# Kernel optimization log

Measured on AMD Instinct MI355X. Metric: run time of the kernel, lower is better.

Reference implementation:

```python
import jax, jax.numpy as jnp
import numpy as np

TAU = 1.0
BETA = 0.1
MIN_NORM = 1.0
B = 4194304


def setup_inputs() -> dict:
    key = jax.random.key(0)
    # positions spread over the four-well landscape (minima near (0.5+-1, 0.5+-1))
    batch = jax.random.normal(key, (B, 2), dtype=jnp.float32) * 1.5
    return {"batch": batch}


def reference(batch):
    batch = batch.reshape(-1, 2)
    u = batch[..., 0] - 0.5
    v = batch[..., 1] - 0.5

    # potential V4 = (u^2-1)^2 + (v^2-1)^2 + beta*u*v
    energy = (u * u - 1.0) ** 2 + (v * v - 1.0) ** 2 + BETA * u * v

    # analytic gradient, forces = -grad
    gx = 4.0 * u * (u * u - 1.0) + BETA * v
    gy = 4.0 * v * (v * v - 1.0) + BETA * u
    forces = -jnp.stack((gx, gy), axis=-1)  # (B, 2)

    # analytic Hessian (B, 2, 2)
    hxx = 12.0 * (u * u) - 4.0
    hyy = 12.0 * (v * v) - 4.0
    hxy = jnp.full_like(hxx, BETA)
    hessian = jnp.stack(
        (jnp.stack((hxx, hxy), axis=-1), jnp.stack((hxy, hyy), axis=-1)), axis=-2
    )

    # eigh: ascending eigenvalues, matching torch.linalg.eigh convention
    eigenvals, eigenvecs = jnp.linalg.eigh(hessian)
    smallest_eigvec = eigenvecs[..., :, 0]  # (B, 2)

    # GAD direction: reflect forces along smallest-eigenvalue eigenvector
    gad = -forces + 2.0 * jnp.sum(forces * smallest_eigvec, axis=-1, keepdims=True) * smallest_eigvec

    # norm_gad_outside_ts branch: normalize gad outside saddle region if small
    eigval_product = eigenvals[..., 0] * eigenvals[..., 1]
    gad_mag = jnp.linalg.norm(gad, axis=-1, keepdims=True)  # (B, 1)
    mask = (eigval_product > 0) & (gad_mag[..., 0] < MIN_NORM)
    gad = jnp.where(mask[..., None], gad / jnp.maximum(gad_mag, 1e-30), gad)

    energy_grad = gad / TAU
    return energy, forces, energy_grad, hessian, eigenvals[..., 0], eigenvals[..., 1]
```

## Files before the change

### kernel.cpp

```cpp
#include <hip/hip_runtime.h>


typedef float f2v __attribute__((ext_vector_type(2)));
typedef float f4v __attribute__((ext_vector_type(4)));

namespace {

__device__ __forceinline__ f2v mk2(float a, float b) {
    f2v r; r.x = a; r.y = b; return r;
}
__device__ __forceinline__ f4v mk4(float a, float b, float c, float d) {
    f4v r; r.x = a; r.y = b; r.z = c; r.w = d; return r;
}

struct PointOut {
    float e, fx, fy, gx, gy, hxx, hyy, l0, l1;
};

__device__ __forceinline__ PointOut compute_point(float px, float py) {
    const float BETA = 0.1f;
    PointOut o;
    float u = px - 0.5f;
    float v = py - 0.5f;
    float uu = u * u;
    float vv = v * v;
    float a = uu - 1.0f;
    float b = vv - 1.0f;

    o.e = a * a + b * b + BETA * u * v;

    float gx = 4.0f * u * a + BETA * v;
    float gy = 4.0f * v * b + BETA * u;
    o.fx = -gx;
    o.fy = -gy;

    o.hxx = 12.0f * uu - 4.0f;
    o.hyy = 12.0f * vv - 4.0f;

    float d = 0.5f * (o.hxx - o.hyy);
    float m = 0.5f * (o.hxx + o.hyy);
    float r = sqrtf(d * d + BETA * BETA);
    o.l0 = m - r;
    o.l1 = m + r;

    bool pos = (d >= 0.0f);
    float wx = pos ? BETA : (d - r);
    float wy = pos ? -(d + r) : BETA;
    float n2 = wx * wx + wy * wy;

    float fd = o.fx * wx + o.fy * wy;
    float s = 2.0f * fd / n2;
    float gadx = -o.fx + s * wx;
    float gady = -o.fy + s * wy;

    float prod = o.l0 * o.l1;
    float gmag = sqrtf(gadx * gadx + gady * gady);
    float scale = (prod > 0.0f && gmag < 1.0f)
                      ? (1.0f / fmaxf(gmag, 1e-30f))
                      : 1.0f;
    o.gx = gadx * scale;
    o.gy = gady * scale;
    return o;
}

}

__global__ __launch_bounds__(256) void fw_energy_gad_kernel(
    const f2v* __restrict__ in, float* __restrict__ out, int n) {
    const float BETA = 0.1f;
    int half = n >> 1;
    size_t N = (size_t)n;
    size_t H = (size_t)half;

    float* e_out  = out;
    f2v*   f_out  = (f2v*)(out + N);
    f2v*   g_out  = (f2v*)(out + 3 * N);
    f4v*   h_out  = (f4v*)(out + 5 * N);
    float* l0_out = out + 9 * N;
    float* l1_out = out + 10 * N;

    int i = blockIdx.x * blockDim.x + threadIdx.x;
    if (i < half) {
        f2v p0 = in[i];
        f2v p1 = in[i + H];
        PointOut o0 = compute_point(p0.x, p0.y);
        PointOut o1 = compute_point(p1.x, p1.y);

        __builtin_nontemporal_store(o0.e, e_out + i);
        __builtin_nontemporal_store(o1.e, e_out + i + H);
        __builtin_nontemporal_store(mk2(o0.fx, o0.fy), f_out + i);
        __builtin_nontemporal_store(mk2(o1.fx, o1.fy), f_out + i + H);
        __builtin_nontemporal_store(mk2(o0.gx, o0.gy), g_out + i);
        __builtin_nontemporal_store(mk2(o1.gx, o1.gy), g_out + i + H);
        __builtin_nontemporal_store(mk4(o0.hxx, BETA, BETA, o0.hyy), h_out + i);
        __builtin_nontemporal_store(mk4(o1.hxx, BETA, BETA, o1.hyy), h_out + i + H);
        __builtin_nontemporal_store(o0.l0, l0_out + i);
        __builtin_nontemporal_store(o1.l0, l0_out + i + H);
        __builtin_nontemporal_store(o0.l1, l1_out + i);
        __builtin_nontemporal_store(o1.l1, l1_out + i + H);
    }

    if ((n & 1) && blockIdx.x == 0 && threadIdx.x == 0) {
        int j = n - 1;
        f2v p = in[j];
        PointOut o = compute_point(p.x, p.y);
        e_out[j]  = o.e;
        f_out[j]  = mk2(o.fx, o.fy);
        g_out[j]  = mk2(o.gx, o.gy);
        h_out[j]  = mk4(o.hxx, BETA, BETA, o.hyy);
        l0_out[j] = o.l0;
        l1_out[j] = o.l1;
    }
}

extern "C" void kernel_launch(void* const* d_in, const int* in_sizes, int n_in,
                              void* d_out, int out_size, void* d_ws, size_t ws_size,
                              hipStream_t stream) {
    const f2v* in = (const f2v*)d_in[0];
    float* out = (float*)d_out;
    int n = in_sizes[0] / 2;

    int half = n >> 1;
    int block = 256;
    int grid = (half + block - 1) / block;
    if (grid < 1) grid = 1;
    fw_energy_gad_kernel<<<grid, block, 0, stream>>>(in, out, n);
}
```

Baseline: 208.3 us.

## Use persistent chunked blocks with wider vector loads, prefetch, and fast math intrinsics

Replaces the one-thread-per-pair launch with a fixed grid of 256 blocks. Each block walks a contiguous chunk, loading two points per thread as a float4 and prefetching two iterations ahead. Outputs are written as wider vectors (float2/float4) with ordinary stores instead of nontemporal ones. The sqrt, division and normalization now use the hardware approximate sqrt, rcp and rsq builtins. The aim is to cut memory instruction count and launch overhead on a bandwidth-bound kernel, at the cost of giving up nontemporal stores, possibly underfilling the GPU with 256 blocks, and a small loss of precision.

```diff
diff --git a/kernel.cpp b/kernel.cpp
--- a/kernel.cpp
+++ b/kernel.cpp
@@ -4,14 +4,10 @@
 typedef float f2v __attribute__((ext_vector_type(2)));
 typedef float f4v __attribute__((ext_vector_type(4)));
 
+#define BLOCK 256
+#define GRID 256
+
 namespace {
-
-__device__ __forceinline__ f2v mk2(float a, float b) {
-    f2v r; r.x = a; r.y = b; return r;
-}
-__device__ __forceinline__ f4v mk4(float a, float b, float c, float d) {
-    f4v r; r.x = a; r.y = b; r.z = c; r.w = d; return r;
-}
 
 struct PointOut {
     float e, fx, fy, gx, gy, hxx, hyy, l0, l1;
@@ -39,7 +35,7 @@
 
     float d = 0.5f * (o.hxx - o.hyy);
     float m = 0.5f * (o.hxx + o.hyy);
-    float r = sqrtf(d * d + BETA * BETA);
+    float r = __builtin_amdgcn_sqrtf(d * d + BETA * BETA);
     o.l0 = m - r;
     o.l1 = m + r;
 
@@ -49,80 +45,107 @@
     float n2 = wx * wx + wy * wy;
 
     float fd = o.fx * wx + o.fy * wy;
-    float s = 2.0f * fd / n2;
+    float s = (2.0f * fd) * __builtin_amdgcn_rcpf(n2);
     float gadx = -o.fx + s * wx;
     float gady = -o.fy + s * wy;
 
     float prod = o.l0 * o.l1;
-    float gmag = sqrtf(gadx * gadx + gady * gady);
-    float scale = (prod > 0.0f && gmag < 1.0f)
-                      ? (1.0f / fmaxf(gmag, 1e-30f))
-                      : 1.0f;
-    o.gx = gadx * scale;
-    o.gy = gady * scale;
+    float g2 = gadx * gadx + gady * gady;
+    if (prod > 0.0f && g2 < 1.0f) {
+        float inv = __builtin_amdgcn_rsqf(fmaxf(g2, 1e-60f));
+        gadx *= inv;
+        gady *= inv;
+    }
+    o.gx = gadx;
+    o.gy = gady;
     return o;
 }
 
 }
 
-__global__ __launch_bounds__(256) void fw_energy_gad_kernel(
+__global__ __launch_bounds__(BLOCK) void fw_chunk_kernel(
+    const f4v* __restrict__ in4, float* __restrict__ out, int n) {
+    const float BETA = 0.1f;
+    int t = threadIdx.x;
+    int np = n >> 1;
+    int ppb = (np + GRID - 1) / GRID;
+    int start = blockIdx.x * ppb;
+    int end   = min(start + ppb, np);
+
+    size_t N = (size_t)n;
+    f2v* e_out  = (f2v*)out;
+    f4v* f_out  = (f4v*)(out + N);
+    f4v* g_out  = (f4v*)(out + 3 * N);
+    f4v* h_out  = (f4v*)(out + 5 * N);
+    f2v* l0_out = (f2v*)(out + 9 * N);
+    f2v* l1_out = (f2v*)(out + 10 * N);
+
+    int j0 = start + t;
+    f4v p0, p1;
+    if (j0 < end)         p0 = in4[j0];
+    if (j0 + BLOCK < end) p1 = in4[j0 + BLOCK];
+
+    for (int j = j0; j < end; j += BLOCK) {
+        int jn = j + 2 * BLOCK;
+        f4v nxt = p0;
+        if (jn < end) nxt = in4[jn];
+
+        f4v cur = p0;
+        p0 = p1;
+        p1 = nxt;
+
+        PointOut o0 = compute_point(cur.x, cur.y);
+        PointOut o1 = compute_point(cur.z, cur.w);
+
+        f2v e; e.x = o0.e; e.y = o1.e;
+        e_out[j] = e;
+        f4v f; f.x = o0.fx; f.y = o0.fy; f.z = o1.fx; f.w = o1.fy;
+        f_out[j] = f;
+        f4v g; g.x = o0.gx; g.y = o0.gy; g.z = o1.gx; g.w = o1.gy;
+        g_out[j] = g;
+        f4v h0; h0.x = o0.hxx; h0.y = BETA; h0.z = BETA; h0.w = o0.hyy;
+        f4v h1; h1.x = o1.hxx; h1.y = BETA; h1.z = BETA; h1.w = o1.hyy;
+        h_out[2 * (size_t)j]     = h0;
+        h_out[2 * (size_t)j + 1] = h1;
+        f2v l0; l0.x = o0.l0; l0.y = o1.l0;
+        l0_out[j] = l0;
+        f2v l1; l1.x = o0.l1; l1.y = o1.l1;
+        l1_out[j] = l1;
+    }
+}
+
+__global__ __launch_bounds__(BLOCK) void fw_energy_gad_scalar(
     const f2v* __restrict__ in, float* __restrict__ out, int n) {
+    int i = blockIdx.x * blockDim.x + threadIdx.x;
+    if (i >= n) return;
     const float BETA = 0.1f;
-    int half = n >> 1;
+    f2v pt = in[i];
+    PointOut o = compute_point(pt.x, pt.y);
     size_t N = (size_t)n;
-    size_t H = (size_t)half;
-
-    float* e_out  = out;
-    f2v*   f_out  = (f2v*)(out + N);
-    f2v*   g_out  = (f2v*)(out + 3 * N);
-    f4v*   h_out  = (f4v*)(out + 5 * N);
-    float* l0_out = out + 9 * N;
-    float* l1_out = out + 10 * N;
-
-    int i = blockIdx.x * blockDim.x + threadIdx.x;
-    if (i < half) {
-        f2v p0 = in[i];
-        f2v p1 = in[i + H];
-        PointOut o0 = compute_point(p0.x, p0.y);
-        PointOut o1 = compute_point(p1.x, p1.y);
-
-        __builtin_nontemporal_store(o0.e, e_out + i);
-        __builtin_nontemporal_store(o1.e, e_out + i + H);
-        __builtin_nontemporal_store(mk2(o0.fx, o0.fy), f_out + i);
-        __builtin_nontemporal_store(mk2(o1.fx, o1.fy), f_out + i + H);
-        __builtin_nontemporal_store(mk2(o0.gx, o0.gy), g_out + i);
-        __builtin_nontemporal_store(mk2(o1.gx, o1.gy), g_out + i + H);
-        __builtin_nontemporal_store(mk4(o0.hxx, BETA, BETA, o0.hyy), h_out + i);
-        __builtin_nontemporal_store(mk4(o1.hxx, BETA, BETA, o1.hyy), h_out + i + H);
-        __builtin_nontemporal_store(o0.l0, l0_out + i);
-        __builtin_nontemporal_store(o1.l0, l0_out + i + H);
-        __builtin_nontemporal_store(o0.l1, l1_out + i);
-        __builtin_nontemporal_store(o1.l1, l1_out + i + H);
-    }
-
-    if ((n & 1) && blockIdx.x == 0 && threadIdx.x == 0) {
-        int j = n - 1;
-        f2v p = in[j];
-        PointOut o = compute_point(p.x, p.y);
-        e_out[j]  = o.e;
-        f_out[j]  = mk2(o.fx, o.fy);
-        g_out[j]  = mk2(o.gx, o.gy);
-        h_out[j]  = mk4(o.hxx, BETA, BETA, o.hyy);
-        l0_out[j] = o.l0;
-        l1_out[j] = o.l1;
-    }
+    out[i] = o.e;
+    f2v fo; fo.x = o.fx; fo.y = o.fy;
+    ((f2v*)(out + N))[i] = fo;
+    f2v go; go.x = o.gx; go.y = o.gy;
+    ((f2v*)(out + 3 * N))[i] = go;
+    out[5 * N + 4 * (size_t)i]     = o.hxx;
+    out[5 * N + 4 * (size_t)i + 1] = BETA;
+    out[5 * N + 4 * (size_t)i + 2] = BETA;
+    out[5 * N + 4 * (size_t)i + 3] = o.hyy;
+    out[9 * N + i]  = o.l0;
+    out[10 * N + i] = o.l1;
 }
 
 extern "C" void kernel_launch(void* const* d_in, const int* in_sizes, int n_in,
                               void* d_out, int out_size, void* d_ws, size_t ws_size,
                               hipStream_t stream) {
-    const f2v* in = (const f2v*)d_in[0];
+    const float* in = (const float*)d_in[0];
     float* out = (float*)d_out;
     int n = in_sizes[0] / 2;
 
-    int half = n >> 1;
-    int block = 256;
-    int grid = (half + block - 1) / block;
-    if (grid < 1) grid = 1;
-    fw_energy_gad_kernel<<<grid, block, 0, stream>>>(in, out, n);
+    if ((n & 3) == 0) {
+        fw_chunk_kernel<<<GRID, BLOCK, 0, stream>>>((const f4v*)in, out, n);
+    } else {
+        int grid = (n + BLOCK - 1) / BLOCK;
+        fw_energy_gad_scalar<<<grid, BLOCK, 0, stream>>>((const f2v*)in, out, n);
+    }
 }
```

Result: slower. 215.6 us (+3.5%).
